# Performance work log

Measured on AMD Instinct MI355X. Metric: run time of the kernel, lower is better.

Reference implementation:

```python
import jax, jax.numpy as jnp
import numpy as np

BN_EPS = 1e-5

def setup_inputs() -> dict:
    key = jax.random.key(0)
    ks = jax.random.split(key, 10)
    B, C, W, H = 4, 128, 32, 128
    Co = C // 2  # 64
    s_in = 1.0 / np.sqrt(C)
    s_out = 1.0 / np.sqrt(Co)
    return {
        "range_x": jax.random.normal(ks[0], (B, C, W, H), jnp.float32),
        "img": jax.random.normal(ks[1], (B, C, W, H), jnp.float32),
        "wq": jax.random.normal(ks[2], (Co, C), jnp.float32) * s_in,
        "bq": jax.random.normal(ks[3], (Co,), jnp.float32) * 0.01,
        "wk": jax.random.normal(ks[4], (Co, C), jnp.float32) * s_in,
        "bk": jax.random.normal(ks[5], (Co,), jnp.float32) * 0.01,
        "wv": jax.random.normal(ks[6], (Co, C), jnp.float32) * s_in,
        "bv": jax.random.normal(ks[7], (Co,), jnp.float32) * 0.01,
        "wc": jax.random.normal(ks[8], (C, Co), jnp.float32) * s_out,
        "bc": jax.random.normal(ks[9], (C,), jnp.float32) * 0.01,
        "bn_gamma": jnp.ones((C,), jnp.float32),
        "bn_beta": jnp.zeros((C,), jnp.float32),
        "bn_mean": jnp.zeros((C,), jnp.float32),
        "bn_var": jnp.ones((C,), jnp.float32),
    }

def reference(range_x, img, wq, bq, wk, bk, wv, bv, wc, bc, bn_gamma, bn_beta, bn_mean, bn_var):
    B, C, W, H = range_x.shape
    HW = W * H
    r = range_x.reshape(B, C, HW)  # [B,C,N]
    i = img.reshape(B, C, HW)
    # 1x1 convs == per-pixel linear projections
    q = jnp.einsum('oc,bcn->bno', wq, r) + bq            # [B,N,Co] (query from range)
    k = jnp.einsum('oc,bcn->bon', wk, i) + bk[None, :, None]  # [B,Co,N]
    corr = jnp.einsum('bno,bom->bnm', q, k)              # [B,N,N]
    attn = jax.nn.softmax(corr, axis=-1)
    v = jnp.einsum('oc,bcn->bon', wv, i) + bv[None, :, None]  # [B,Co,N]
    # out[b,o,n] = sum_m v[b,o,m] * attn[b,n,m]  (bmm(V, attn^T))
    out = jnp.einsum('bom,bnm->bon', v, attn)            # [B,Co,N]
    # channel_back: 1x1 conv -> BN (inference) -> ReLU
    y = jnp.einsum('co,bon->bcn', wc, out) + bc[None, :, None]
    inv = bn_gamma / jnp.sqrt(bn_var + BN_EPS)
    y = y * inv[None, :, None] + (bn_beta - bn_mean * inv)[None, :, None]
    y = jax.nn.relu(y)
    return img + y.reshape(B, C, W, H)
```

## Files before the change

kernel.cpp:

```cpp
#include <hip/hip_runtime.h>
#include <hip/hip_bf16.h>

typedef __attribute__((ext_vector_type(4))) float f32x4;
typedef __attribute__((ext_vector_type(8))) short s16x8;
typedef __attribute__((ext_vector_type(4))) short s16x4;

#define LOG2E 1.4426950408889634f

__device__ __forceinline__ ushort f2bf(float f){
  union { __hip_bfloat16 h; ushort u; } c;
  c.h = __float2bfloat16(f);
  return c.u;
}
__device__ __forceinline__ float bf2f(ushort h){
  union { unsigned u; float f; } x; x.u = ((unsigned)h) << 16;
  return x.f;
}

__device__ __forceinline__ void gload16(const void* g, void* l){
  __builtin_amdgcn_global_load_lds(
      (const __attribute__((address_space(1))) void*)g,
      (__attribute__((address_space(3))) void*)l, 16, 0, 0);
}

#if __has_builtin(__builtin_amdgcn_mfma_f32_16x16x16bf16_1k)
__device__ __forceinline__ f32x4 mfma16(s16x4 a, s16x4 b, f32x4 c){
  return __builtin_amdgcn_mfma_f32_16x16x16bf16_1k(a, b, c, 0, 0, 0);
}
#elif __has_builtin(__builtin_amdgcn_mfma_f32_16x16x16_bf16)
__device__ __forceinline__ f32x4 mfma16(s16x4 a, s16x4 b, f32x4 c){
  return __builtin_amdgcn_mfma_f32_16x16x16_bf16(a, b, c, 0, 0, 0);
}
#else
__device__ __forceinline__ f32x4 mfma16(s16x4 a, s16x4 b, f32x4 c){
  f32x4 d;
  asm volatile("v_mfma_f32_16x16x16_bf16 %0, %1, %2, %3\n\ts_nop 7\n\ts_nop 7"
               : "=v"(d) : "v"(a), "v"(b), "v"(c));
  return d;
}
#endif

__global__ __launch_bounds__(256) void wprep(
    const float* __restrict__ wq, const float* __restrict__ wk,
    const float* __restrict__ wv, ushort* __restrict__ Wh,
    ushort* __restrict__ Wl)
{
  int flat = blockIdx.x*256 + threadIdx.x;
  int row = flat >> 7, c = flat & 127;
  float v = (row < 64) ? wq[row*128 + c]
          : (row < 128) ? wk[(row-64)*128 + c]
          : wv[(row-128)*128 + c];
  ushort hi = f2bf(v);
  Wh[flat] = hi;
  Wl[flat] = f2bf(v - bf2f(hi));
}

__global__ __launch_bounds__(256, 2) void proj_qkv(
    const float* __restrict__ xr, const float* __restrict__ xi,
    const ushort* __restrict__ Wh, const ushort* __restrict__ Wl,
    const float* __restrict__ bq, const float* __restrict__ bk,
    const float* __restrict__ bv,
    ushort* __restrict__ Qh, ushort* __restrict__ Ql,
    ushort* __restrict__ Kh, ushort* __restrict__ Vt)
{
  __shared__ __align__(16) float xrL[128*64];
  __shared__ __align__(16) float xiL[128*64];
  const int tid = threadIdx.x;
  const int idx = blockIdx.x;
  const int oh  = idx & 1;
  const int nt  = (idx >> 1) & 63;
  const int b   = idx >> 7;
  const int n0  = nt << 6;
  const int lane = tid & 63;
  const int w    = tid >> 6;
  const int l15  = lane & 15;
  const int g    = lane >> 4;

  {
    const float* xrs = xr + (size_t)b*524288 + n0;
    const float* xis = xi + (size_t)b*524288 + n0;
    #pragma unroll
    for (int j = 0; j < 8; ++j){
      int row = j*16 + (tid >> 4);
      int ch  = tid & 15;
      gload16(xrs + (size_t)row*4096 + ch*4, xrL + j*1024 + w*256);
      gload16(xis + (size_t)row*4096 + ch*4, xiL + j*1024 + w*256);
    }
  }
  __syncthreads();

  s16x8 xrh[4], xrl[4], xih[4], xil[4];
  const int px = w*16 + l15;
  #pragma unroll
  for (int kc = 0; kc < 4; ++kc){
    #pragma unroll
    for (int j = 0; j < 8; ++j){
      int r = kc*32 + g*8 + j;
      float a = xrL[r*64 + px];
      ushort h = f2bf(a);
      xrh[kc][j] = (short)h;
      xrl[kc][j] = (short)f2bf(a - bf2f(h));
      float bb = xiL[r*64 + px];
      ushort h2 = f2bf(bb);
      xih[kc][j] = (short)h2;
      xil[kc][j] = (short)f2bf(bb - bf2f(h2));
    }
  }

  #pragma unroll
  for (int ot = 0; ot < 6; ++ot){
    const int p    = ot >> 1;
    const int sub  = ot & 1;
    const int obase = oh*32 + sub*16;
    const int wrow  = p*64 + obase;
    f32x4 acc = {0.f,0.f,0.f,0.f};
    #pragma unroll
    for (int kc = 0; kc < 4; ++kc){
      s16x8 whf = *(const s16x8*)(Wh + (size_t)(wrow + l15)*128 + kc*32 + g*8);
      s16x8 wlf = *(const s16x8*)(Wl + (size_t)(wrow + l15)*128 + kc*32 + g*8);
      const s16x8 xh = (p==0) ? xrh[kc] : xih[kc];
      const s16x8 xl = (p==0) ? xrl[kc] : xil[kc];
      if (p < 2){
        acc = __builtin_amdgcn_mfma_f32_16x16x32_bf16(xh, whf, acc, 0,0,0);
        acc = __builtin_amdgcn_mfma_f32_16x16x32_bf16(xl, whf, acc, 0,0,0);
        acc = __builtin_amdgcn_mfma_f32_16x16x32_bf16(xh, wlf, acc, 0,0,0);
      } else {
        acc = __builtin_amdgcn_mfma_f32_16x16x32_bf16(whf, xh, acc, 0,0,0);
        acc = __builtin_amdgcn_mfma_f32_16x16x32_bf16(wlf, xh, acc, 0,0,0);
        acc = __builtin_amdgcn_mfma_f32_16x16x32_bf16(whf, xl, acc, 0,0,0);
      }
    }
    if (p == 0){
      float bqv = bq[obase + l15];
      #pragma unroll
      for (int r = 0; r < 4; ++r){
        float q = (acc[r] + bqv) * LOG2E;
        ushort hi = f2bf(q);
        size_t a = (size_t)(b*4096 + n0 + w*16 + g*4 + r)*64 + obase + l15;
        Qh[a] = hi; Ql[a] = f2bf(q - bf2f(hi));
      }
    } else if (p == 1){
      float bkv = bk[obase + l15];
      #pragma unroll
      for (int r = 0; r < 4; ++r){
        float k = acc[r] + bkv;
        size_t a = (size_t)(b*4096 + n0 + w*16 + g*4 + r)*64 + obase + l15;
        Kh[a] = f2bf(k);
      }
    } else {
      #pragma unroll
      for (int r = 0; r < 4; ++r){
        int o = obase + g*4 + r;
        float v = acc[r] + bv[o];
        Vt[(size_t)(b*64 + o)*4096 + n0 + w*16 + l15] = f2bf(v);
      }
    }
  }
}

__global__ __launch_bounds__(256, 5) void flash_attn(
    const ushort* __restrict__ Qh, const ushort* __restrict__ Ql,
    const ushort* __restrict__ Kh, const ushort* __restrict__ Vt,
    float* __restrict__ Opart, float* __restrict__ Mst,
    float* __restrict__ Lst)
{
  __shared__ __align__(16) ushort khL[2][4096];
  __shared__ __align__(16) ushort vL[2][4096];

  const int tid  = threadIdx.x;
  const int idx  = blockIdx.x;
  const int ks   = idx & 3;
  const int qt   = (idx >> 2) & 63;
  const int b    = idx >> 8;
  const int lane = tid & 63;
  const int w    = tid >> 6;
  const int l15  = lane & 15;
  const int g    = lane >> 4;
  const int qrow = qt*64 + w*16;
  const int kv0  = ks << 10;
  const int srow = lane >> 2;
  const int sg   = lane & 3;
  const int sgs  = sg ^ ((srow >> 1) & 3);

  const size_t qoff = ((size_t)(b*4096 + qrow + l15))*64 + g*8;
  s16x8 qh0 = *(const s16x8*)(Qh + qoff);
  s16x8 qh1 = *(const s16x8*)(Qh + qoff + 32);
  s16x8 ql0 = *(const s16x8*)(Ql + qoff);
  s16x8 ql1 = *(const s16x8*)(Ql + qoff + 32);

  const char* KhB = (const char*)(Kh + (size_t)b*4096*64);
  const char* VB  = (const char*)(Vt + (size_t)b*64*4096);

  s16x4 ones4;
  #pragma unroll
  for (int e=0;e<4;++e) ones4[e] = (short)0x3F80;

  f32x4 o_acc[4];
  #pragma unroll
  for (int ot=0;ot<4;++ot) o_acc[ot] = (f32x4){0.f,0.f,0.f,0.f};
  f32x4 sum_acc = {0.f,0.f,0.f,0.f};
  float m_run = -1e30f;

  #define STAGE_KV(kvb, bi)                                               \
  {                                                                       \
    size_t kr = (size_t)((kvb) + w*16 + srow)*128 + sgs*16;               \
    char* kd = (char*)khL[bi] + w*2048;                                   \
    gload16(KhB + kr,      kd);                                           \
    gload16(KhB + kr + 64, kd + 1024);                                    \
    size_t vr = (size_t)(w*16 + srow)*8192 + (size_t)(kvb)*2 + sgs*16;    \
    char* vd = (char*)vL[bi] + w*2048;                                    \
    gload16(VB + vr,      vd);                                            \
    gload16(VB + vr + 64, vd + 1024);                                     \
  }

  STAGE_KV(kv0, 0);
  __syncthreads();

  const int swz = (l15 >> 1) & 3;
  const int kfrag = l15*64 + (g ^ swz)*16;

  for (int t = 0; t < 16; ++t){
    const int cb = t & 1;

    if (t < 15){
      STAGE_KV(kv0 + (t+1)*64, cb ^ 1);
    }

    f32x4 s[4];
    __builtin_amdgcn_s_setprio(1);
    #pragma unroll
    for (int ct=0; ct<4; ++ct){
      const char* kb = (const char*)khL[cb] + ct*2048;
      s16x8 kh0 = *(const s16x8*)(kb + kfrag);
      s16x8 kh1 = *(const s16x8*)(kb + 1024 + kfrag);
      f32x4 acc = {0.f,0.f,0.f,0.f};
      acc = __builtin_amdgcn_mfma_f32_16x16x32_bf16(kh0, ql0, acc, 0, 0, 0);
      acc = __builtin_amdgcn_mfma_f32_16x16x32_bf16(kh1, ql1, acc, 0, 0, 0);
      acc = __builtin_amdgcn_mfma_f32_16x16x32_bf16(kh0, qh0, acc, 0, 0, 0);
      acc = __builtin_amdgcn_mfma_f32_16x16x32_bf16(kh1, qh1, acc, 0, 0, 0);
      s[ct] = acc;
    }
    __builtin_amdgcn_s_setprio(0);

    float mx = fmaxf(
        fmaxf(fmaxf(fmaxf(s[0][0],s[0][1]), fmaxf(s[0][2],s[0][3])),
              fmaxf(fmaxf(s[1][0],s[1][1]), fmaxf(s[1][2],s[1][3]))),
        fmaxf(fmaxf(fmaxf(s[2][0],s[2][1]), fmaxf(s[2][2],s[2][3])),
              fmaxf(fmaxf(s[3][0],s[3][1]), fmaxf(s[3][2],s[3][3]))));
    mx = fmaxf(mx, __shfl_xor(mx, 16));
    mx = fmaxf(mx, __shfl_xor(mx, 32));
    if (!__all(mx <= m_run + 8.0f)){
      float mn = fmaxf(m_run, mx);
      float sc = exp2f(m_run - mn);
      m_run = mn;
      #pragma unroll
      for (int ot=0;ot<4;++ot) o_acc[ot] *= sc;
      sum_acc *= sc;
    }
    s16x4 pbf[4];
    #pragma unroll
    for (int ct=0;ct<4;++ct){
      #pragma unroll
      for (int r=0;r<4;++r){
        pbf[ct][r] = (short)f2bf(exp2f(s[ct][r] - m_run));
      }
    }

    __builtin_amdgcn_s_setprio(1);
    #pragma unroll
    for (int ct=0; ct<4; ++ct)
      sum_acc = mfma16(ones4, pbf[ct], sum_acc);
    #pragma unroll
    for (int ot=0; ot<4; ++ot){
      const char* vbase = (const char*)vL[cb] + ot*2048 + l15*64;
      #pragma unroll
      for (int ct=0; ct<4; ++ct){
        int chunk = (((ct & 1) << 1) + (g >> 1)) ^ swz;
        s16x4 av = *(const s16x4*)(vbase + (ct>>1)*1024 + chunk*16 + (g&1)*8);
        o_acc[ot] = mfma16(av, pbf[ct], o_acc[ot]);
      }
    }
    __builtin_amdgcn_s_setprio(0);

    __syncthreads();
  }
  #undef STAGE_KV

  float* ep = (float*)((char*)vL + (size_t)w*4096);
  #pragma unroll
  for (int ot=0;ot<4;++ot){
    int dw = l15*64 + ((ot*16 + g*4) ^ ((l15 & 7) << 2));
    *(f32x4*)(ep + dw) = o_acc[ot];
  }
  __syncthreads();
  {
    const int q4  = lane >> 2;
    const int seg = lane & 3;
    float* Ob = Opart + ((size_t)(ks*4 + b)*4096 + qrow)*64;
    #pragma unroll
    for (int c=0;c<4;++c){
      int o0 = seg*16 + c*4;
      f32x4 vv = *(const f32x4*)(ep + q4*64 + (o0 ^ ((q4 & 7) << 2)));
      *(f32x4*)(Ob + (size_t)q4*64 + o0) = vv;
    }
  }
  if (lane < 16){
    Mst[(size_t)(ks*4 + b)*4096 + qrow + lane] = m_run;
    Lst[(size_t)(ks*4 + b)*4096 + qrow + lane] = sum_acc[0];
  }
}

__global__ __launch_bounds__(256) void final_proj(
    const float* __restrict__ Opart, const float* __restrict__ Mst,
    const float* __restrict__ Lst, const float* __restrict__ wc,
    const float* __restrict__ bc, const float* __restrict__ gm,
    const float* __restrict__ bt, const float* __restrict__ mu,
    const float* __restrict__ vr, const float* __restrict__ img,
    float* __restrict__ out)
{
  __shared__ float ol[64*64];
  __shared__ float scl[4][64];
  const int tid = threadIdx.x;
  const int idx = blockIdx.x;
  const int cs  = idx & 3;
  const int nt  = (idx >> 2) & 63;
  const int b   = idx >> 8;
  const int n0  = nt << 6;

  if (tid < 64){
    size_t rid = (size_t)b*4096 + n0 + tid;
    float m0 = Mst[0*16384 + rid], m1 = Mst[1*16384 + rid];
    float m2 = Mst[2*16384 + rid], m3 = Mst[3*16384 + rid];
    float mm = fmaxf(fmaxf(m0,m1), fmaxf(m2,m3));
    float s0 = exp2f(m0-mm), s1 = exp2f(m1-mm);
    float s2 = exp2f(m2-mm), s3 = exp2f(m3-mm);
    float li = s0*Lst[0*16384+rid] + s1*Lst[1*16384+rid]
             + s2*Lst[2*16384+rid] + s3*Lst[3*16384+rid];
    float inv = 1.0f / li;
    scl[0][tid] = s0*inv; scl[1][tid] = s1*inv;
    scl[2][tid] = s2*inv; scl[3][tid] = s3*inv;
  }
  __syncthreads();

  {
    const size_t base = ((size_t)b*4096 + n0)*64;
    for (int j=0;j<16;++j){
      int flat = tid + (j << 8);
      int n = flat >> 6, o = flat & 63;
      float v = Opart[0*(size_t)16384*64 + base + flat] * scl[0][n]
              + Opart[1*(size_t)16384*64 + base + flat] * scl[1][n]
              + Opart[2*(size_t)16384*64 + base + flat] * scl[2][n]
              + Opart[3*(size_t)16384*64 + base + flat] * scl[3][n];
      ol[(o << 6) + (n ^ (o & 31))] = v;
    }
  }
  __syncthreads();

  const int lane = tid & 63;
  const int w = __builtin_amdgcn_readfirstlane(tid >> 6);
  const int c0 = (cs << 5) + (w << 3);

  float acc[8];
  #pragma unroll
  for (int cc=0;cc<8;++cc) acc[cc] = 0.f;

  for (int o=0;o<64;++o){
    float v = ol[(o << 6) + (lane ^ (o & 31))];
    #pragma unroll
    for (int cc=0;cc<8;++cc)
      acc[cc] = fmaf(wc[(c0+cc)*64 + o], v, acc[cc]);
  }

  #pragma unroll
  for (int cc=0;cc<8;++cc){
    int c = c0 + cc;
    float inv = gm[c] * rsqrtf(vr[c] + 1e-5f);
    float sh  = bt[c] - mu[c]*inv;
    float y = (acc[cc] + bc[c]) * inv + sh;
    y = fmaxf(y, 0.f);
    size_t gi = ((size_t)(b*128 + c))*4096 + n0 + lane;
    out[gi] = img[gi] + y;
  }
}

extern "C" void kernel_launch(void* const* d_in, const int* in_sizes, int n_in,
                              void* d_out, int out_size, void* d_ws, size_t ws_size,
                              hipStream_t stream)
{
  const float* xr = (const float*)d_in[0];
  const float* xi = (const float*)d_in[1];
  const float* wq = (const float*)d_in[2];
  const float* bq = (const float*)d_in[3];
  const float* wk = (const float*)d_in[4];
  const float* bk = (const float*)d_in[5];
  const float* wv = (const float*)d_in[6];
  const float* bv = (const float*)d_in[7];
  const float* wc = (const float*)d_in[8];
  const float* bc = (const float*)d_in[9];
  const float* gm = (const float*)d_in[10];
  const float* bt = (const float*)d_in[11];
  const float* mu = (const float*)d_in[12];
  const float* vr = (const float*)d_in[13];
  float* out = (float*)d_out;

  const size_t SZ = (size_t)4*4096*64;
  ushort* Qhw = (ushort*)d_ws;
  ushort* Qlw = Qhw + SZ;
  ushort* Khw = Qlw + SZ;
  ushort* Vtw = Khw + SZ;
  float*  Ow  = (float*)(Vtw + SZ);
  float*  Mw  = Ow + (size_t)16*4096*64;
  float*  Lw  = Mw + (size_t)16*4096;
  ushort* Whb = (ushort*)(Lw + (size_t)16*4096);
  ushort* Wlb = Whb + 192*128;

  wprep     <<<96,   256, 0, stream>>>(wq, wk, wv, Whb, Wlb);
  proj_qkv  <<<512,  256, 0, stream>>>(xr, xi, Whb, Wlb, bq, bk, bv,
                                       Qhw, Qlw, Khw, Vtw);
  flash_attn<<<1024, 256, 0, stream>>>(Qhw, Qlw, Khw, Vtw, Ow, Mw, Lw);
  final_proj<<<1024, 256, 0, stream>>>(Ow, Mw, Lw, wc, bc, gm, bt, mu, vr, xi, out);
}
```

Measured before the change: 95.62 us.

## Software-pipeline QK^T one tile ahead with triple-buffered K staging

Restructures the flash-attention loop so the QK^T MFMAs for the next KV tile are issued before the softmax and PV of the current tile. K is now staged two tiles ahead into a triple-buffered LDS ring and V one tile ahead. The aim is to overlap the exp/max VALU work with matrix-core work and hide load latency. In exchange it uses more LDS and registers (s_next), so launch bounds drop from 5 to 4 blocks per CU. Float-to-bf16 conversion is also replaced with a manual round-to-nearest-even bit trick, and the row-sum MFMAs move after the PV MFMAs.

```diff
diff --git a/kernel.cpp b/kernel.cpp
--- a/kernel.cpp
+++ b/kernel.cpp
@@ -8,9 +8,9 @@
 #define LOG2E 1.4426950408889634f
 
 __device__ __forceinline__ ushort f2bf(float f){
-  union { __hip_bfloat16 h; ushort u; } c;
-  c.h = __float2bfloat16(f);
-  return c.u;
+  union { float f; unsigned u; } x; x.f = f;
+  unsigned r = x.u + 0x7fffu + ((x.u >> 16) & 1u);
+  return (ushort)(r >> 16);
 }
 __device__ __forceinline__ float bf2f(ushort h){
   union { unsigned u; float f; } x; x.u = ((unsigned)h) << 16;
@@ -158,13 +158,13 @@
   }
 }
 
-__global__ __launch_bounds__(256, 5) void flash_attn(
+__global__ __launch_bounds__(256, 4) void flash_attn(
     const ushort* __restrict__ Qh, const ushort* __restrict__ Ql,
     const ushort* __restrict__ Kh, const ushort* __restrict__ Vt,
     float* __restrict__ Opart, float* __restrict__ Mst,
     float* __restrict__ Lst)
 {
-  __shared__ __align__(16) ushort khL[2][4096];
+  __shared__ __align__(16) ushort khL[3][4096];
   __shared__ __align__(16) ushort vL[2][4096];
 
   const int tid  = threadIdx.x;
@@ -201,52 +201,59 @@
   f32x4 sum_acc = {0.f,0.f,0.f,0.f};
   float m_run = -1e30f;
 
-  #define STAGE_KV(kvb, bi)                                               \
+  #define STAGE_K(kvb, bi)                                                \
   {                                                                       \
     size_t kr = (size_t)((kvb) + w*16 + srow)*128 + sgs*16;               \
     char* kd = (char*)khL[bi] + w*2048;                                   \
     gload16(KhB + kr,      kd);                                           \
     gload16(KhB + kr + 64, kd + 1024);                                    \
+  }
+  #define STAGE_V(kvb, bi)                                                \
+  {                                                                       \
     size_t vr = (size_t)(w*16 + srow)*8192 + (size_t)(kvb)*2 + sgs*16;    \
     char* vd = (char*)vL[bi] + w*2048;                                    \
     gload16(VB + vr,      vd);                                            \
     gload16(VB + vr + 64, vd + 1024);                                     \
   }
 
-  STAGE_KV(kv0, 0);
+  STAGE_K(kv0, 0);
+  STAGE_V(kv0, 0);
+  STAGE_K(kv0 + 64, 1);
   __syncthreads();
 
   const int swz = (l15 >> 1) & 3;
   const int kfrag = l15*64 + (g ^ swz)*16;
 
+  #define QK_TILE(dst, bi)                                                \
+  {                                                                       \
+    _Pragma("unroll")                                                     \
+    for (int ct=0; ct<4; ++ct){                                           \
+      const char* kb = (const char*)khL[bi] + ct*2048;                    \
+      s16x8 kh0 = *(const s16x8*)(kb + kfrag);                            \
+      s16x8 kh1 = *(const s16x8*)(kb + 1024 + kfrag);                     \
+      f32x4 acc = {0.f,0.f,0.f,0.f};                                      \
+      acc = __builtin_amdgcn_mfma_f32_16x16x32_bf16(kh0, ql0, acc,0,0,0); \
+      acc = __builtin_amdgcn_mfma_f32_16x16x32_bf16(kh1, ql1, acc,0,0,0); \
+      acc = __builtin_amdgcn_mfma_f32_16x16x32_bf16(kh0, qh0, acc,0,0,0); \
+      acc = __builtin_amdgcn_mfma_f32_16x16x32_bf16(kh1, qh1, acc,0,0,0); \
+      dst[ct] = acc;                                                      \
+    }                                                                     \
+  }
+
+  f32x4 s_cur[4], s_next[4];
+  QK_TILE(s_cur, 0);
+
   for (int t = 0; t < 16; ++t){
-    const int cb = t & 1;
-
-    if (t < 15){
-      STAGE_KV(kv0 + (t+1)*64, cb ^ 1);
-    }
-
-    f32x4 s[4];
-    __builtin_amdgcn_s_setprio(1);
-    #pragma unroll
-    for (int ct=0; ct<4; ++ct){
-      const char* kb = (const char*)khL[cb] + ct*2048;
-      s16x8 kh0 = *(const s16x8*)(kb + kfrag);
-      s16x8 kh1 = *(const s16x8*)(kb + 1024 + kfrag);
-      f32x4 acc = {0.f,0.f,0.f,0.f};
-      acc = __builtin_amdgcn_mfma_f32_16x16x32_bf16(kh0, ql0, acc, 0, 0, 0);
-      acc = __builtin_amdgcn_mfma_f32_16x16x32_bf16(kh1, ql1, acc, 0, 0, 0);
-      acc = __builtin_amdgcn_mfma_f32_16x16x32_bf16(kh0, qh0, acc, 0, 0, 0);
-      acc = __builtin_amdgcn_mfma_f32_16x16x32_bf16(kh1, qh1, acc, 0, 0, 0);
-      s[ct] = acc;
-    }
-    __builtin_amdgcn_s_setprio(0);
+    if (t < 15) STAGE_V(kv0 + (t+1)*64, (t+1) & 1);
+    if (t < 14) STAGE_K(kv0 + (t+2)*64, (t+2) % 3);
+
+    if (t < 15) QK_TILE(s_next, (t+1) % 3);
 
     float mx = fmaxf(
-        fmaxf(fmaxf(fmaxf(s[0][0],s[0][1]), fmaxf(s[0][2],s[0][3])),
-              fmaxf(fmaxf(s[1][0],s[1][1]), fmaxf(s[1][2],s[1][3]))),
-        fmaxf(fmaxf(fmaxf(s[2][0],s[2][1]), fmaxf(s[2][2],s[2][3])),
-              fmaxf(fmaxf(s[3][0],s[3][1]), fmaxf(s[3][2],s[3][3]))));
+        fmaxf(fmaxf(fmaxf(s_cur[0][0],s_cur[0][1]), fmaxf(s_cur[0][2],s_cur[0][3])),
+              fmaxf(fmaxf(s_cur[1][0],s_cur[1][1]), fmaxf(s_cur[1][2],s_cur[1][3]))),
+        fmaxf(fmaxf(fmaxf(s_cur[2][0],s_cur[2][1]), fmaxf(s_cur[2][2],s_cur[2][3])),
+              fmaxf(fmaxf(s_cur[3][0],s_cur[3][1]), fmaxf(s_cur[3][2],s_cur[3][3]))));
     mx = fmaxf(mx, __shfl_xor(mx, 16));
     mx = fmaxf(mx, __shfl_xor(mx, 32));
     if (!__all(mx <= m_run + 8.0f)){
@@ -262,14 +269,12 @@
     for (int ct=0;ct<4;++ct){
       #pragma unroll
       for (int r=0;r<4;++r){
-        pbf[ct][r] = (short)f2bf(exp2f(s[ct][r] - m_run));
+        pbf[ct][r] = (short)f2bf(exp2f(s_cur[ct][r] - m_run));
       }
     }
 
     __builtin_amdgcn_s_setprio(1);
-    #pragma unroll
-    for (int ct=0; ct<4; ++ct)
-      sum_acc = mfma16(ones4, pbf[ct], sum_acc);
+    const int cb = t & 1;
     #pragma unroll
     for (int ot=0; ot<4; ++ot){
       const char* vbase = (const char*)vL[cb] + ot*2048 + l15*64;
@@ -280,11 +285,19 @@
         o_acc[ot] = mfma16(av, pbf[ct], o_acc[ot]);
       }
     }
+    #pragma unroll
+    for (int ct=0; ct<4; ++ct)
+      sum_acc = mfma16(ones4, pbf[ct], sum_acc);
     __builtin_amdgcn_s_setprio(0);
 
     __syncthreads();
-  }
-  #undef STAGE_KV
+
+    #pragma unroll
+    for (int ct=0; ct<4; ++ct) s_cur[ct] = s_next[ct];
+  }
+  #undef STAGE_K
+  #undef STAGE_V
+  #undef QK_TILE
 
   float* ep = (float*)((char*)vL + (size_t)w*4096);
   #pragma unroll
```

After: 96.43 us. No clear change (+0.8%).
